# Kernel optimization log

Measured on AMD Instinct MI355X. Metric: run time of the kernel, lower is better.

## Reference

```python
import jax, jax.numpy as jnp
import numpy as np

B, S, SKV = 16, 4096, 77      # CFG batch (8+8), latent tokens 64x64, CLIP text tokens
HID, CDIM, HEADS = 1280, 768, 8


def setup_inputs() -> dict:
    key = jax.random.key(0)
    ks = jax.random.split(key, 7)
    return {
        "hidden_states": jax.random.normal(ks[0], (B, S, HID), jnp.float32),
        "encoder_hidden_states": jax.random.normal(ks[1], (B, SKV, CDIM), jnp.float32),
        "Wq": jax.random.normal(ks[2], (HID, HID), jnp.float32) * 0.02,
        "Wk": jax.random.normal(ks[3], (HID, CDIM), jnp.float32) * 0.02,
        "Wv": jax.random.normal(ks[4], (HID, CDIM), jnp.float32) * 0.02,
        "Wo": jax.random.normal(ks[5], (HID, HID), jnp.float32) * 0.02,
        "bo": jnp.zeros((HID,), jnp.float32),
        "heads": HEADS,
    }


def reference(hidden_states, encoder_hidden_states, Wq, Wk, Wv, Wo, bo, heads):
    b, s, hid = hidden_states.shape
    d = hid // heads  # head dim
    scale = 1.0 / jnp.sqrt(jnp.asarray(d, hidden_states.dtype))

    q = hidden_states @ Wq.T                      # [B, S, HID]
    k = encoder_hidden_states @ Wk.T              # [B, SKV, HID]
    v = encoder_hidden_states @ Wv.T

    # crossattn detach trick: first text token of k/v is detached (forward identity)
    k = jnp.concatenate([jax.lax.stop_gradient(k[:, :1]), k[:, 1:]], axis=1)
    v = jnp.concatenate([jax.lax.stop_gradient(v[:, :1]), v[:, 1:]], axis=1)

    qh = q.reshape(b, s, heads, d)
    kh = k.reshape(b, -1, heads, d)
    vh = v.reshape(b, -1, heads, d)

    scores = jnp.einsum('bqhd,bkhd->bhqk', qh, kh) * scale   # [B, H, S, SKV]
    probs = jax.nn.softmax(scores, axis=-1)
    out = jnp.einsum('bhqk,bkhd->bqhd', probs, vh).reshape(b, s, hid)

    return out @ Wo.T + bo  # dropout p=0.0 is identity
```

## Files before the change

kernel.cpp:

```cpp
#include <hip/hip_runtime.h>
#include <stdint.h>
#include <cmath>

typedef unsigned short u16;
typedef _Float16 f16;
typedef f16   f16x8 __attribute__((ext_vector_type(8)));
typedef float f32x4 __attribute__((ext_vector_type(4)));
typedef u16   u16x8 __attribute__((ext_vector_type(8)));

#define GLD16(gsrc, ldst)                                                      \
  __builtin_amdgcn_global_load_lds(                                            \
      (__attribute__((address_space(1))) void*)(gsrc),                         \
      (__attribute__((address_space(3))) void*)(ldst), 16, 0, 0)

__device__ __forceinline__ u16 f2h(float x) {
  f16 h = (f16)x;
  return __builtin_bit_cast(u16, h);
}

__device__ __forceinline__ f32x4 mfma16(f16x8 a, f16x8 b, f32x4 c) {
  return __builtin_amdgcn_mfma_f32_16x16x32_f16(a, b, c, 0, 0, 0);
}

__global__ void cvt_f32_f16(const float* __restrict__ in, u16* __restrict__ out,
                            long n8) {
  long i = (long)blockIdx.x * 256 + threadIdx.x;
  const long stride = (long)gridDim.x * 256;
  for (; i < n8; i += stride) {
    const float4* p = (const float4*)in + 2 * i;
    float4 a = p[0], b = p[1];
    u16x8 o;
    o[0] = f2h(a.x); o[1] = f2h(a.y); o[2] = f2h(a.z); o[3] = f2h(a.w);
    o[4] = f2h(b.x); o[5] = f2h(b.y); o[6] = f2h(b.z); o[7] = f2h(b.w);
    *((u16x8*)out + i) = o;
  }
}

__device__ __forceinline__ void xcd_tile(int& m0, int& n0, int N) {
  int nwg = gridDim.x;
  int orig = blockIdx.x;
  int q8 = nwg >> 3, r8 = nwg & 7;
  int xcd = orig & 7, idx = orig >> 3;
  int wg = (xcd < r8 ? xcd * (q8 + 1) : r8 * (q8 + 1) + (xcd - r8) * q8) + idx;
  const int gn = N >> 8;
  m0 = (wg / gn) * 256;
  n0 = (wg % gn) * 256;
}

__global__ __launch_bounds__(512, 2) void gemm_a32(const float* __restrict__ A,
                                                   const u16* __restrict__ B,
                                                   u16* __restrict__ C,
                                                   int M, int N, int K) {
  extern __shared__ char smem[];
  const int tid = threadIdx.x;
  const int lane = tid & 63, wid = tid >> 6;
  const int wm = wid >> 2, wn = wid & 3;
  const int lq = lane >> 4, lr = lane & 15;

  int m0, n0;
  xcd_tile(m0, n0, N);
  const int NT = K >> 6;

  const int r0 = tid >> 3;
  const float* pA = A + (size_t)(m0 + r0) * K + (tid & 7) * 8;
  const int dcolA = (((tid & 7) ^ (r0 & 7)) << 4);

  const int kb0 = (((tid & 7) ^ ((tid >> 3) & 7)) << 4);
  const u16* pB = B + (size_t)(n0 + r0) * K + (kb0 >> 1);

#define ALOAD(DST, TT)                                                        \
  do {                                                                        \
    const float* s_ = pA + (size_t)(TT) * 64;                                 \
    _Pragma("unroll") for (int j = 0; j < 4; ++j) {                           \
      DST[2 * j]     = *(const float4*)(s_ + (size_t)(64 * j) * K);           \
      DST[2 * j + 1] = *(const float4*)(s_ + (size_t)(64 * j) * K + 4);       \
    }                                                                         \
  } while (0)

#define AWRITE(SRC, TT)                                                       \
  do {                                                                        \
    char* db_ = smem + ((TT) & 1) * 65536;                                    \
    _Pragma("unroll") for (int j = 0; j < 4; ++j) {                           \
      u16x8 w_;                                                               \
      w_[0] = f2h(SRC[2 * j].x);     w_[1] = f2h(SRC[2 * j].y);               \
      w_[2] = f2h(SRC[2 * j].z);     w_[3] = f2h(SRC[2 * j].w);               \
      w_[4] = f2h(SRC[2 * j + 1].x); w_[5] = f2h(SRC[2 * j + 1].y);           \
      w_[6] = f2h(SRC[2 * j + 1].z); w_[7] = f2h(SRC[2 * j + 1].w);           \
      *(u16x8*)(db_ + (r0 + 64 * j) * 128 + dcolA) = w_;                      \
    }                                                                         \
  } while (0)

#define STAGEB(HALF, TT)                                                      \
  do {                                                                        \
    char* db_ = smem + ((TT) & 1) * 65536 + 32768 + (HALF) * 16384 +          \
                wid * 1024;                                                   \
    const u16* s_ = pB + (size_t)((HALF) * 128) * K + (size_t)(TT) * 64;      \
    GLD16(s_, db_);                                                           \
    GLD16(s_ + (size_t)64 * K, db_ + 8192);                                   \
  } while (0)

  int kx[2];
#pragma unroll
  for (int ks = 0; ks < 2; ++ks)
    kx[ks] = ((ks * 64 + lq * 16) ^ ((lr & 7) << 4));
  const int ABASE = wm * 8192 + lr * 128;
  const int BBASE = 32768 + wn * 4096 + lr * 128;

#define READA(FA, QM)                                                         \
  _Pragma("unroll") for (int m2 = 0; m2 < 4; ++m2)                            \
  _Pragma("unroll") for (int ks = 0; ks < 2; ++ks)                            \
    FA[m2][ks] = *(const f16x8*)(rb + ABASE + (QM) * 16384 + m2 * 2048 + kx[ks]);
#define READB(FB, QN)                                                         \
  _Pragma("unroll") for (int n2 = 0; n2 < 2; ++n2)                            \
  _Pragma("unroll") for (int ks = 0; ks < 2; ++ks)                            \
    FB[n2][ks] = *(const f16x8*)(rb + BBASE + (QN) * 16384 + n2 * 2048 + kx[ks]);
#define CLUSTER(QM, QN, FA, FB)                                               \
  __builtin_amdgcn_s_setprio(1);                                              \
  _Pragma("unroll") for (int m2 = 0; m2 < 4; ++m2)                            \
  _Pragma("unroll") for (int n2 = 0; n2 < 2; ++n2)                            \
  _Pragma("unroll") for (int ks = 0; ks < 2; ++ks)                            \
      acc[QM][QN][m2][n2] =                                                   \
          mfma16(FA[m2][ks], FB[n2][ks], acc[QM][QN][m2][n2]);                \
  __builtin_amdgcn_s_setprio(0);

  f32x4 acc[2][2][4][2] = {};
  float4 a4[8], a4n[8];

  ALOAD(a4, 0);
  STAGEB(0, 0);
  STAGEB(1, 0);
  asm volatile("" ::: "memory");
  AWRITE(a4, 0);
  ALOAD(a4n, 1);
  asm volatile("s_waitcnt vmcnt(8)" ::: "memory");
  asm volatile("s_waitcnt lgkmcnt(0)" ::: "memory");
  __builtin_amdgcn_s_barrier();

  for (int t = 0; t < NT; ++t) {
    const char* rb = smem + (t & 1) * 65536;
    f16x8 fa[4][2], fb0[2][2], fb1[2][2];
    READA(fa, 0);
    READB(fb0, 0);
    CLUSTER(0, 0, fa, fb0);
    READA(fa, 1);
    CLUSTER(1, 0, fa, fb0);
    READB(fb1, 1);
    CLUSTER(1, 1, fa, fb1);
    READA(fa, 0);
    CLUSTER(0, 1, fa, fb1);
    if (t + 1 < NT) {
      STAGEB(0, t + 1);
      STAGEB(1, t + 1);
      asm volatile("" ::: "memory");
      AWRITE(a4n, t + 1);
      if (t + 2 < NT) {
        ALOAD(a4n, t + 2);
        asm volatile("s_waitcnt vmcnt(8)" ::: "memory");
      } else {
        asm volatile("s_waitcnt vmcnt(0)" ::: "memory");
      }
      asm volatile("s_waitcnt lgkmcnt(0)" ::: "memory");
      __builtin_amdgcn_s_barrier();
    }
  }
#undef ALOAD
#undef AWRITE
#undef STAGEB
#undef READA
#undef READB
#undef CLUSTER

#pragma unroll
  for (int qm = 0; qm < 2; ++qm)
#pragma unroll
    for (int m2 = 0; m2 < 4; ++m2)
#pragma unroll
      for (int r = 0; r < 4; ++r) {
        int grow = m0 + qm * 128 + wm * 64 + m2 * 16 + lq * 4 + r;
#pragma unroll
        for (int qn = 0; qn < 2; ++qn)
#pragma unroll
          for (int n2 = 0; n2 < 2; ++n2) {
            int gcol = n0 + qn * 128 + wn * 32 + n2 * 16 + lr;
            C[(size_t)grow * N + gcol] = f2h(acc[qm][qn][m2][n2][r]);
          }
      }
}

template <int OUT_F16, int HAS_BIAS>
__global__ __launch_bounds__(512, 2) void gemm_8ph(const u16* __restrict__ A,
                                                   const u16* __restrict__ B,
                                                   void* __restrict__ Cp,
                                                   const float* __restrict__ bias,
                                                   int M, int N, int K) {
  extern __shared__ char smem[];
  const int tid = threadIdx.x;
  const int lane = tid & 63, wid = tid >> 6;
  const int wm = wid >> 2, wn = wid & 3;
  const int lq = lane >> 4, lr = lane & 15;

  int m0, n0;
  xcd_tile(m0, n0, N);
  const int NT = K >> 6;

  const int r0 = tid >> 3;
  const int kb0 = (((tid & 7) ^ ((tid >> 3) & 7)) << 4);
  const u16* pA = A + (size_t)(m0 + r0) * K + (kb0 >> 1);
  const u16* pB = B + (size_t)(n0 + r0) * K + (kb0 >> 1);

#define STAGE(MAT, HALF, TT)                                                  \
  do {                                                                        \
    char* db_ = smem + ((TT) & 1) * 65536 + (MAT) * 32768 +                   \
                (HALF) * 16384 + wid * 1024;                                  \
    const u16* s_ = (MAT ? pB : pA) + (size_t)((HALF) * 128) * K +            \
                    (size_t)(TT) * 64;                                        \
    GLD16(s_, db_);                                                           \
    GLD16(s_ + (size_t)64 * K, db_ + 8192);                                   \
  } while (0)

  int kx[2];
#pragma unroll
  for (int ks = 0; ks < 2; ++ks)
    kx[ks] = ((ks * 64 + lq * 16) ^ ((lr & 7) << 4));
  const int ABASE = wm * 8192 + lr * 128;
  const int BBASE = 32768 + wn * 4096 + lr * 128;

#define READA(FA, QM)                                                         \
  _Pragma("unroll") for (int m2 = 0; m2 < 4; ++m2)                            \
  _Pragma("unroll") for (int ks = 0; ks < 2; ++ks)                            \
    FA[m2][ks] = *(const f16x8*)(rb + ABASE + (QM) * 16384 + m2 * 2048 + kx[ks]);
#define READB(FB, QN)                                                         \
  _Pragma("unroll") for (int n2 = 0; n2 < 2; ++n2)                            \
  _Pragma("unroll") for (int ks = 0; ks < 2; ++ks)                            \
    FB[n2][ks] = *(const f16x8*)(rb + BBASE + (QN) * 16384 + n2 * 2048 + kx[ks]);
#define CLUSTER(QM, QN, FA, FB)                                               \
  __builtin_amdgcn_s_setprio(1);                                              \
  _Pragma("unroll") for (int m2 = 0; m2 < 4; ++m2)                            \
  _Pragma("unroll") for (int n2 = 0; n2 < 2; ++n2)                            \
  _Pragma("unroll") for (int ks = 0; ks < 2; ++ks)                            \
      acc[QM][QN][m2][n2] =                                                   \
          mfma16(FA[m2][ks], FB[n2][ks], acc[QM][QN][m2][n2]);                \
  __builtin_amdgcn_s_setprio(0);

  f32x4 acc[2][2][4][2] = {};

  STAGE(0, 0, 0);
  STAGE(1, 0, 0);
  STAGE(0, 1, 0);
  STAGE(1, 1, 0);
  asm volatile("s_waitcnt vmcnt(0)" ::: "memory");
  __builtin_amdgcn_s_barrier();

  for (int t = 0; t < NT; ++t) {
    const char* rb = smem + (t & 1) * 65536;
    f16x8 fa0[4][2], fa1[4][2], fb0[2][2], fb1[2][2];
    READA(fa0, 0);
    READB(fb0, 0);
    if (t + 1 < NT) {
      STAGE(0, 0, t + 1);
      asm volatile("s_waitcnt vmcnt(4)" ::: "memory");
    } else {
      asm volatile("s_waitcnt vmcnt(2)" ::: "memory");
    }
    __builtin_amdgcn_s_barrier();
    asm volatile("s_waitcnt lgkmcnt(0)" ::: "memory");
    CLUSTER(0, 0, fa0, fb0);
    __builtin_amdgcn_s_barrier();
    READA(fa1, 1);
    if (t + 1 < NT) {
      STAGE(1, 0, t + 1);
      asm volatile("s_waitcnt vmcnt(4)" ::: "memory");
    } else {
      asm volatile("s_waitcnt vmcnt(0)" ::: "memory");
    }
    __builtin_amdgcn_s_barrier();
    asm volatile("s_waitcnt lgkmcnt(0)" ::: "memory");
    CLUSTER(1, 0, fa1, fb0);
    __builtin_amdgcn_s_barrier();
    READB(fb1, 1);
    if (t + 1 < NT) STAGE(0, 1, t + 1);
    __builtin_amdgcn_s_barrier();
    asm volatile("s_waitcnt lgkmcnt(0)" ::: "memory");
    CLUSTER(1, 1, fa1, fb1);
    __builtin_amdgcn_s_barrier();
    READA(fa0, 0);
    if (t + 1 < NT) {
      STAGE(1, 1, t + 1);
      asm volatile("s_waitcnt vmcnt(4)" ::: "memory");
    }
    __builtin_amdgcn_s_barrier();
    asm volatile("s_waitcnt lgkmcnt(0)" ::: "memory");
    CLUSTER(0, 1, fa0, fb1);
    __builtin_amdgcn_s_barrier();
  }
#undef STAGE
#undef READA
#undef READB
#undef CLUSTER

  float bv[2][2];
#pragma unroll
  for (int qn = 0; qn < 2; ++qn)
#pragma unroll
    for (int n2 = 0; n2 < 2; ++n2)
      bv[qn][n2] =
          HAS_BIAS ? bias[n0 + qn * 128 + wn * 32 + n2 * 16 + lr] : 0.0f;
#pragma unroll
  for (int qm = 0; qm < 2; ++qm)
#pragma unroll
    for (int m2 = 0; m2 < 4; ++m2)
#pragma unroll
      for (int r = 0; r < 4; ++r) {
        int grow = m0 + qm * 128 + wm * 64 + m2 * 16 + lq * 4 + r;
#pragma unroll
        for (int qn = 0; qn < 2; ++qn)
#pragma unroll
          for (int n2 = 0; n2 < 2; ++n2) {
            int gcol = n0 + qn * 128 + wn * 32 + n2 * 16 + lr;
            float v = acc[qm][qn][m2][n2][r] + bv[qn][n2];
            if (OUT_F16)
              ((u16*)Cp)[(size_t)grow * N + gcol] = f2h(v);
            else
              ((float*)Cp)[(size_t)grow * N + gcol] = v;
          }
      }
}

template <int OUT_F16, int HAS_BIAS, int MTAIL>
__global__ __launch_bounds__(256) void gemm_bt(const u16* __restrict__ A,
                                               const u16* __restrict__ B,
                                               void* __restrict__ Cp,
                                               const float* __restrict__ bias,
                                               int M, int N, int K) {
  constexpr int BK = 64;
  __shared__ u16 Asm[128 * BK];
  __shared__ u16 Bsm[128 * BK];
  const int tid = threadIdx.x;
  const int lane = tid & 63, wid = tid >> 6;
  const int wm = wid >> 1, wn = wid & 1;
  const int m0 = blockIdx.y * 128, n0 = blockIdx.x * 128;
  const int lq = lane >> 4, lr = lane & 15;
  const int koff = lq << 3;

  f32x4 acc[4][4] = {};

  for (int k0 = 0; k0 < K; k0 += BK) {
#pragma unroll
    for (int j = 0; j < 4; ++j) {
      int off = (wid * 4 + j) * 1024 + lane * 16;
      int r = off >> 7;
      int c = (off & 127) >> 1;
      int gr = m0 + r;
      if (MTAIL) gr = gr < M ? gr : M - 1;
      GLD16(A + (size_t)gr * K + k0 + c, (char*)Asm + (wid * 4 + j) * 1024);
    }
#pragma unroll
    for (int j = 0; j < 4; ++j) {
      int off = (wid * 4 + j) * 1024 + lane * 16;
      int r = off >> 7;
      int c = (off & 127) >> 1;
      GLD16(B + (size_t)(n0 + r) * K + k0 + c, (char*)Bsm + (wid * 4 + j) * 1024);
    }
    __syncthreads();
#pragma unroll
    for (int ks = 0; ks < 2; ++ks) {
      f16x8 af[4], bfr[4];
#pragma unroll
      for (int m = 0; m < 4; ++m)
        af[m] = *(const f16x8*)(Asm + (wm * 64 + m * 16 + lr) * BK + ks * 32 + koff);
#pragma unroll
      for (int n = 0; n < 4; ++n)
        bfr[n] = *(const f16x8*)(Bsm + (wn * 64 + n * 16 + lr) * BK + ks * 32 + koff);
#pragma unroll
      for (int m = 0; m < 4; ++m)
#pragma unroll
        for (int n = 0; n < 4; ++n)
          acc[m][n] = mfma16(af[m], bfr[n], acc[m][n]);
    }
    __syncthreads();
  }

#pragma unroll
  for (int m = 0; m < 4; ++m) {
#pragma unroll
    for (int r = 0; r < 4; ++r) {
      int grow = m0 + wm * 64 + m * 16 + lq * 4 + r;
      if (MTAIL && grow >= M) continue;
#pragma unroll
      for (int n = 0; n < 4; ++n) {
        int gcol = n0 + wn * 64 + n * 16 + lr;
        float v = acc[m][n][r];
        if (HAS_BIAS) v += bias[gcol];
        if (OUT_F16)
          ((u16*)Cp)[(size_t)grow * N + gcol] = f2h(v);
        else
          ((float*)Cp)[(size_t)grow * N + gcol] = v;
      }
    }
  }
}

__global__ __launch_bounds__(256) void attn_fused(const u16* __restrict__ Q,
                                                  const u16* __restrict__ Kp,
                                                  const u16* __restrict__ Vp,
                                                  u16* __restrict__ Oa,
                                                  float scale) {
  __shared__ u16 Ksm[80][168];
  __shared__ u16 VT[160][104];
  __shared__ u16 Psm[4][16][96];
  const int tid = threadIdx.x, lane = tid & 63, wid = tid >> 6;
  const int lq = lane >> 4, lr = lane & 15, koff = lq << 3;
  const int qg = blockIdx.x, h = blockIdx.y, b = blockIdx.z;

  {
    u16x8 z = {0, 0, 0, 0, 0, 0, 0, 0};
    for (int i = tid; i < 80 * 168 / 8; i += 256) ((u16x8*)&Ksm[0][0])[i] = z;
    for (int i = tid; i < 160 * 104 / 8; i += 256) ((u16x8*)&VT[0][0])[i] = z;
    for (int i = tid; i < 4 * 16 * 96 / 8; i += 256) ((u16x8*)&Psm[0][0][0])[i] = z;
  }
  __syncthreads();

  const size_t kvbase = ((size_t)b * 77) * 1280 + (size_t)h * 160;
  for (int i = tid; i < 77 * 20; i += 256) {
    int r = i / 20, c8 = (i % 20) * 8;
    *(u16x8*)&Ksm[r][c8] = *(const u16x8*)(Kp + kvbase + (size_t)r * 1280 + c8);
  }
  for (int i = tid; i < 77 * 20; i += 256) {
    int r = i / 20, c8 = (i % 20) * 8;
    u16x8 v = *(const u16x8*)(Vp + kvbase + (size_t)r * 1280 + c8);
#pragma unroll
    for (int j = 0; j < 8; ++j) VT[c8 + j][r] = v[j];
  }
  __syncthreads();

  for (int it = 0; it < 4; ++it) {
    const int qt = qg * 4 + it;

    f16x8 qf[5];
    const int qrow = qt * 64 + wid * 16 + lr;
    const size_t qbase = ((size_t)b * 4096 + qrow) * 1280 + (size_t)h * 160;
#pragma unroll
    for (int ks = 0; ks < 5; ++ks)
      qf[ks] = *(const f16x8*)(Q + qbase + ks * 32 + koff);

    f32x4 sc[5];
#pragma unroll
    for (int nt = 0; nt < 5; ++nt) {
      sc[nt] = (f32x4){0.f, 0.f, 0.f, 0.f};
#pragma unroll
      for (int ks = 0; ks < 5; ++ks) {
        f16x8 kf = *(const f16x8*)&Ksm[nt * 16 + lr][ks * 32 + koff];
        sc[nt] = mfma16(qf[ks], kf, sc[nt]);
      }
    }

    float p[5][4];
#pragma unroll
    for (int r = 0; r < 4; ++r) {
      float mx = -1e30f;
#pragma unroll
      for (int nt = 0; nt < 5; ++nt) {
        float v = sc[nt][r] * scale;
        if (nt * 16 + lr >= 77) v = -1e30f;
        p[nt][r] = v;
        mx = fmaxf(mx, v);
      }
#pragma unroll
      for (int d = 1; d < 16; d <<= 1) mx = fmaxf(mx, __shfl_xor(mx, d));
      float sum = 0.f;
#pragma unroll
      for (int nt = 0; nt < 5; ++nt) {
        float e = __expf(p[nt][r] - mx);
        p[nt][r] = e;
        sum += e;
      }
#pragma unroll
      for (int d = 1; d < 16; d <<= 1) sum += __shfl_xor(sum, d);
      float inv = 1.f / sum;
#pragma unroll
      for (int nt = 0; nt < 5; ++nt) p[nt][r] *= inv;
    }

#pragma unroll
    for (int r = 0; r < 4; ++r)
#pragma unroll
      for (int nt = 0; nt < 5; ++nt)
        Psm[wid][lq * 4 + r][nt * 16 + lr] = f2h(p[nt][r]);

    f32x4 ov[10];
#pragma unroll
    for (int n2 = 0; n2 < 10; ++n2) ov[n2] = (f32x4){0.f, 0.f, 0.f, 0.f};
#pragma unroll
    for (int k2 = 0; k2 < 3; ++k2) {
      f16x8 pf = *(const f16x8*)&Psm[wid][lr][k2 * 32 + koff];
#pragma unroll
      for (int n2 = 0; n2 < 10; ++n2) {
        f16x8 vf = *(const f16x8*)&VT[n2 * 16 + lr][k2 * 32 + koff];
        ov[n2] = mfma16(pf, vf, ov[n2]);
      }
    }

    const size_t ob = ((size_t)b * 4096 + (size_t)qt * 64 + wid * 16) * 1280 +
                      (size_t)h * 160;
#pragma unroll
    for (int c = 0; c < 2; ++c) {
#pragma unroll
      for (int r = 0; r < 4; ++r)
#pragma unroll
        for (int n2l = 0; n2l < 5; ++n2l)
          Psm[wid][lq * 4 + r][n2l * 16 + lr] = f2h(ov[c * 5 + n2l][r]);
#pragma unroll
      for (int u0 = 0; u0 < 3; ++u0) {
        int u = lane + u0 * 64;
        if (u < 160) {
          int rr = u / 10, cc = u - rr * 10;
          u16x8 v = *(const u16x8*)&Psm[wid][rr][cc * 8];
          *(u16x8*)(Oa + ob + (size_t)rr * 1280 + c * 80 + cc * 8) = v;
        }
      }
    }
  }
}

extern "C" void kernel_launch(void* const* d_in, const int* in_sizes, int n_in,
                              void* d_out, int out_size, void* d_ws,
                              size_t ws_size, hipStream_t stream) {
  (void)in_sizes; (void)n_in; (void)out_size; (void)ws_size;
  const float* hs  = (const float*)d_in[0];
  const float* enc = (const float*)d_in[1];
  const float* Wq  = (const float*)d_in[2];
  const float* Wk  = (const float*)d_in[3];
  const float* Wv  = (const float*)d_in[4];
  const float* Wo  = (const float*)d_in[5];
  const float* bo  = (const float*)d_in[6];
  float* out = (float*)d_out;

  const int B = 16, S = 4096, SKV = 77, HID = 1280, CDIM = 768;
  const int MQ = B * S;
  const int MKV = B * SKV;

  char* ws = (char*)d_ws;
  size_t off = 0;
  auto alloc = [&](size_t bytes) -> char* {
    char* p = ws + off;
    off += (bytes + 255) & ~(size_t)255;
    return p;
  };
  u16* q_h    = (u16*)alloc((size_t)MQ * HID * 2);
  u16* attn_h = (u16*)alloc((size_t)MQ * HID * 2);
  u16* enc_h  = (u16*)alloc((size_t)MKV * CDIM * 2);
  u16* wq_h   = (u16*)alloc((size_t)HID * HID * 2);
  u16* wk_h   = (u16*)alloc((size_t)HID * CDIM * 2);
  u16* wv_h   = (u16*)alloc((size_t)HID * CDIM * 2);
  u16* wo_h   = (u16*)alloc((size_t)HID * HID * 2);
  u16* k_h    = (u16*)alloc((size_t)MKV * HID * 2);
  u16* v_h    = (u16*)alloc((size_t)MKV * HID * 2);

  auto cvt = [&](const float* src, u16* dst, long n) {
    long n8 = n / 8;
    int blocks = (int)((n8 + 255) / 256);
    if (blocks > 2048) blocks = 2048;
    cvt_f32_f16<<<blocks, 256, 0, stream>>>(src, dst, n8);
  };
  cvt(enc, enc_h, (long)MKV * CDIM);
  cvt(Wq,  wq_h,  (long)HID * HID);
  cvt(Wk,  wk_h,  (long)HID * CDIM);
  cvt(Wv,  wv_h,  (long)HID * CDIM);
  cvt(Wo,  wo_h,  (long)HID * HID);

  gemm_bt<1, 0, 1><<<dim3(10, 10), 256, 0, stream>>>(enc_h, wk_h, k_h, nullptr, MKV, HID, CDIM);
  gemm_bt<1, 0, 1><<<dim3(10, 10), 256, 0, stream>>>(enc_h, wv_h, v_h, nullptr, MKV, HID, CDIM);

  const int grid_big = (MQ / 256) * (HID / 256);
  gemm_a32<<<dim3(grid_big), dim3(512), 131072, stream>>>(
      hs, wq_h, q_h, MQ, HID, HID);

  const float scale = 1.0f / sqrtf(160.0f);
  attn_fused<<<dim3(16, 8, 16), 256, 0, stream>>>(q_h, k_h, v_h, attn_h, scale);

  gemm_8ph<0, 1><<<dim3(grid_big), dim3(512), 131072, stream>>>(
      attn_h, wo_h, out, bo, MQ, HID, HID);
}
```

Before: 690.4 us.

## Merge conversion and K/V GEMM launches, keep A fragments in registers

The five fp32-to-fp16 conversion launches become one multi-segment kernel, and the separate K and V projection GEMMs become a single launch with a doubled grid that picks the weight and output per block. In both big GEMM main loops the A fragments for the first k-half now stay in registers, so the re-read of LDS before the last MFMA cluster is gone. This trims launch overhead and LDS traffic, but holding the extra fragment raises register pressure in kernels launched with two blocks per CU.

New measurement: 863.2 us. 1.25x slower.

```diff
diff --git a/kernel.cpp b/kernel.cpp
--- a/kernel.cpp
+++ b/kernel.cpp
@@ -22,17 +22,29 @@
   return __builtin_amdgcn_mfma_f32_16x16x32_f16(a, b, c, 0, 0, 0);
 }
 
-__global__ void cvt_f32_f16(const float* __restrict__ in, u16* __restrict__ out,
-                            long n8) {
+__global__ void cvt_multi(const float* __restrict__ s0, u16* __restrict__ d0, long c0,
+                          const float* __restrict__ s1, u16* __restrict__ d1, long c1,
+                          const float* __restrict__ s2, u16* __restrict__ d2, long c2,
+                          const float* __restrict__ s3, u16* __restrict__ d3, long c3,
+                          const float* __restrict__ s4, u16* __restrict__ d4, long c4) {
   long i = (long)blockIdx.x * 256 + threadIdx.x;
   const long stride = (long)gridDim.x * 256;
-  for (; i < n8; i += stride) {
-    const float4* p = (const float4*)in + 2 * i;
+  for (; i < c4; i += stride) {
+    const float* s;
+    u16* d;
+    long base;
+    if (i < c0)      { s = s0; d = d0; base = 0;  }
+    else if (i < c1) { s = s1; d = d1; base = c0; }
+    else if (i < c2) { s = s2; d = d2; base = c1; }
+    else if (i < c3) { s = s3; d = d3; base = c2; }
+    else             { s = s4; d = d4; base = c3; }
+    long j = i - base;
+    const float4* p = (const float4*)s + 2 * j;
     float4 a = p[0], b = p[1];
     u16x8 o;
     o[0] = f2h(a.x); o[1] = f2h(a.y); o[2] = f2h(a.z); o[3] = f2h(a.w);
     o[4] = f2h(b.x); o[5] = f2h(b.y); o[6] = f2h(b.z); o[7] = f2h(b.w);
-    *((u16x8*)out + i) = o;
+    *((u16x8*)d + j) = o;
   }
 }
 
@@ -138,16 +150,15 @@
 
   for (int t = 0; t < NT; ++t) {
     const char* rb = smem + (t & 1) * 65536;
-    f16x8 fa[4][2], fb0[2][2], fb1[2][2];
-    READA(fa, 0);
+    f16x8 fa0[4][2], fa1[4][2], fb0[2][2], fb1[2][2];
+    READA(fa0, 0);
     READB(fb0, 0);
-    CLUSTER(0, 0, fa, fb0);
-    READA(fa, 1);
-    CLUSTER(1, 0, fa, fb0);
+    CLUSTER(0, 0, fa0, fb0);
+    READA(fa1, 1);
+    CLUSTER(1, 0, fa1, fb0);
     READB(fb1, 1);
-    CLUSTER(1, 1, fa, fb1);
-    READA(fa, 0);
-    CLUSTER(0, 1, fa, fb1);
+    CLUSTER(1, 1, fa1, fb1);
+    CLUSTER(0, 1, fa0, fb1);
     if (t + 1 < NT) {
       STAGEB(0, t + 1);
       STAGEB(1, t + 1);
@@ -283,7 +294,6 @@
     asm volatile("s_waitcnt lgkmcnt(0)" ::: "memory");
     CLUSTER(1, 1, fa1, fb1);
     __builtin_amdgcn_s_barrier();
-    READA(fa0, 0);
     if (t + 1 < NT) {
       STAGE(1, 1, t + 1);
       asm volatile("s_waitcnt vmcnt(4)" ::: "memory");
@@ -326,11 +336,11 @@
       }
 }
 
-template <int OUT_F16, int HAS_BIAS, int MTAIL>
-__global__ __launch_bounds__(256) void gemm_bt(const u16* __restrict__ A,
-                                               const u16* __restrict__ B,
-                                               void* __restrict__ Cp,
-                                               const float* __restrict__ bias,
+__global__ __launch_bounds__(256) void gemm_kv(const u16* __restrict__ A,
+                                               const u16* __restrict__ Bk,
+                                               const u16* __restrict__ Bv,
+                                               u16* __restrict__ Ck,
+                                               u16* __restrict__ Cv,
                                                int M, int N, int K) {
   constexpr int BK = 64;
   __shared__ u16 Asm[128 * BK];
@@ -338,7 +348,12 @@
   const int tid = threadIdx.x;
   const int lane = tid & 63, wid = tid >> 6;
   const int wm = wid >> 1, wn = wid & 1;
-  const int m0 = blockIdx.y * 128, n0 = blockIdx.x * 128;
+  int nx = blockIdx.x;
+  const u16* B;
+  u16* C;
+  if (nx >= 10) { B = Bv; C = Cv; nx -= 10; }
+  else          { B = Bk; C = Ck; }
+  const int m0 = blockIdx.y * 128, n0 = nx * 128;
   const int lq = lane >> 4, lr = lane & 15;
   const int koff = lq << 3;
 
@@ -351,7 +366,7 @@
       int r = off >> 7;
       int c = (off & 127) >> 1;
       int gr = m0 + r;
-      if (MTAIL) gr = gr < M ? gr : M - 1;
+      gr = gr < M ? gr : M - 1;
       GLD16(A + (size_t)gr * K + k0 + c, (char*)Asm + (wid * 4 + j) * 1024);
     }
 #pragma unroll
@@ -385,16 +400,11 @@
 #pragma unroll
     for (int r = 0; r < 4; ++r) {
       int grow = m0 + wm * 64 + m * 16 + lq * 4 + r;
-      if (MTAIL && grow >= M) continue;
+      if (grow >= M) continue;
 #pragma unroll
       for (int n = 0; n < 4; ++n) {
         int gcol = n0 + wn * 64 + n * 16 + lr;
-        float v = acc[m][n][r];
-        if (HAS_BIAS) v += bias[gcol];
-        if (OUT_F16)
-          ((u16*)Cp)[(size_t)grow * N + gcol] = f2h(v);
-        else
-          ((float*)Cp)[(size_t)grow * N + gcol] = v;
+        C[(size_t)grow * N + gcol] = f2h(acc[m][n][r]);
       }
     }
   }
@@ -556,20 +566,20 @@
   u16* k_h    = (u16*)alloc((size_t)MKV * HID * 2);
   u16* v_h    = (u16*)alloc((size_t)MKV * HID * 2);
 
-  auto cvt = [&](const float* src, u16* dst, long n) {
-    long n8 = n / 8;
-    int blocks = (int)((n8 + 255) / 256);
-    if (blocks > 2048) blocks = 2048;
-    cvt_f32_f16<<<blocks, 256, 0, stream>>>(src, dst, n8);
-  };
-  cvt(enc, enc_h, (long)MKV * CDIM);
-  cvt(Wq,  wq_h,  (long)HID * HID);
-  cvt(Wk,  wk_h,  (long)HID * CDIM);
-  cvt(Wv,  wv_h,  (long)HID * CDIM);
-  cvt(Wo,  wo_h,  (long)HID * HID);
-
-  gemm_bt<1, 0, 1><<<dim3(10, 10), 256, 0, stream>>>(enc_h, wk_h, k_h, nullptr, MKV, HID, CDIM);
-  gemm_bt<1, 0, 1><<<dim3(10, 10), 256, 0, stream>>>(enc_h, wv_h, v_h, nullptr, MKV, HID, CDIM);
+  const long n8_enc = (long)MKV * CDIM / 8;
+  const long n8_wq  = (long)HID * HID / 8;
+  const long n8_wk  = (long)HID * CDIM / 8;
+  const long c0 = n8_enc;
+  const long c1 = c0 + n8_wq;
+  const long c2 = c1 + n8_wk;
+  const long c3 = c2 + n8_wk;
+  const long c4 = c3 + n8_wq;
+  cvt_multi<<<2048, 256, 0, stream>>>(enc, enc_h, c0, Wq, wq_h, c1,
+                                      Wk, wk_h, c2, Wv, wv_h, c3,
+                                      Wo, wo_h, c4);
+
+  gemm_kv<<<dim3(20, 10), 256, 0, stream>>>(enc_h, wk_h, wv_h, k_h, v_h,
+                                            MKV, HID, CDIM);
 
   const int grid_big = (MQ / 256) * (HID / 256);
   gemm_a32<<<dim3(grid_big), dim3(512), 131072, stream>>>(
```
